# Optimization experiments

Hardware: AMD Instinct MI355X
Metric: run time of the kernel (lower is better)

## Reference

```python
import jax, jax.numpy as jnp
import numpy as np

D_MODEL = 1024
N_HEADS = 16
D_K = D_MODEL // N_HEADS
CAUSAL = True


def setup_inputs() -> dict:
    key = jax.random.key(0)
    ks = jax.random.split(key, 11)
    B, S, D = 2, 2048, D_MODEL
    scale = 1.0 / np.sqrt(D)
    inp = {
        "in_Q": jax.random.normal(ks[0], (B, S, D), jnp.float32),
        "in_K": jax.random.normal(ks[1], (B, S, D), jnp.float32),
        "in_V": jax.random.normal(ks[2], (B, S, D), jnp.float32),
        # torch Linear params: weight [out, in], bias [out]
        "Wq": jax.random.normal(ks[3], (D, D), jnp.float32) * scale,
        "bq": jax.random.normal(ks[4], (D,), jnp.float32) * scale,
        "Wk": jax.random.normal(ks[5], (D, D), jnp.float32) * scale,
        "bk": jax.random.normal(ks[6], (D,), jnp.float32) * scale,
        "Wv": jax.random.normal(ks[7], (D, D), jnp.float32) * scale,
        "bv": jax.random.normal(ks[8], (D,), jnp.float32) * scale,
        "Wo": jax.random.normal(ks[9], (D, D), jnp.float32) * scale,
        "bo": jax.random.normal(ks[10], (D,), jnp.float32) * scale,
    }
    return inp


def reference(in_Q, in_K, in_V, Wq, bq, Wk, bk, Wv, bv, Wo, bo):
    B, S, D = in_Q.shape
    H, dk = N_HEADS, D_K
    # Linear projections (torch: x @ W.T + b)
    Q = in_Q @ Wq.T + bq
    K = in_K @ Wk.T + bk
    V = in_V @ Wv.T + bv
    # split heads: [B, S, D] -> [B, H, S, dk]
    Qh = Q.reshape(B, S, H, dk).transpose(0, 2, 1, 3)
    Kh = K.reshape(B, S, H, dk).transpose(0, 2, 1, 3)
    Vh = V.reshape(B, S, H, dk).transpose(0, 2, 1, 3)
    # scores [B, H, S, S]
    scores = jnp.einsum("bhqd,bhkd->bhqk", Qh, Kh) / jnp.sqrt(jnp.float32(dk))
    if CAUSAL:
        mask = jnp.tril(jnp.ones((S, S), dtype=bool))
        scores = jnp.where(mask, scores, -jnp.inf)
    attn = jax.nn.softmax(scores, axis=-1)
    out = jnp.einsum("bhqk,bhkd->bhqd", attn, Vh)
    Hcat = out.transpose(0, 2, 1, 3).reshape(B, S, D)
    return Hcat @ Wo.T + bo
```

## Files before the change

kernel.cpp:

```cpp
#include <hip/hip_runtime.h>
#include <hip/hip_bf16.h>
#include <math.h>

#define D_MODEL 1024
#define NHEADS  16
#define DK      64
#define SEQ     2048
#define BATCH   2
#define MROWS   4096
#define NQT     (SEQ/64)

typedef unsigned short ushort_t;
using short8 = __attribute__((ext_vector_type(8))) short;
using f32x4  = __attribute__((ext_vector_type(4))) float;

__device__ __forceinline__ ushort_t f2bf(float x) {
    unsigned u = __float_as_uint(x);
    u = (u + 0x7FFFu + ((u >> 16) & 1u)) >> 16;
    return (ushort_t)u;
}

__device__ __forceinline__ unsigned pk2(float a, float b) {
    __hip_bfloat162 h = __float22bfloat162_rn(float2{a, b});
    unsigned u;
    __builtin_memcpy(&u, &h, 4);
    return u;
}

__device__ __forceinline__ void gll16(const ushort_t* g, ushort_t* l) {
    __builtin_amdgcn_global_load_lds(
        (const __attribute__((address_space(1))) void*)(g),
        (__attribute__((address_space(3))) void*)(l), 16, 0, 0);
}

__global__ __launch_bounds__(256) void cvt_bf16(
    const float* s0, const float* s1, const float* s2, const float* s3,
    const float* s4, const float* s5, const float* s6,
    ushort_t* d0, ushort_t* d1, ushort_t* d2, ushort_t* d3,
    ushort_t* d4, ushort_t* d5, ushort_t* d6, int nIn, int nW)
{
    const float* s; ushort_t* d; int n;
    switch (blockIdx.y) {
        case 0: s = s0; d = d0; n = nIn; break;
        case 1: s = s1; d = d1; n = nIn; break;
        case 2: s = s2; d = d2; n = nIn; break;
        case 3: s = s3; d = d3; n = nW;  break;
        case 4: s = s4; d = d4; n = nW;  break;
        case 5: s = s5; d = d5; n = nW;  break;
        default: s = s6; d = d6; n = nW; break;
    }
    int i = (blockIdx.x * 256 + threadIdx.x) * 4;
    if (i < n) {
        float4 v = *(const float4*)&s[i];
        ushort4 o;
        o.x = f2bf(v.x); o.y = f2bf(v.y); o.z = f2bf(v.z); o.w = f2bf(v.w);
        *(ushort4*)&d[i] = o;
    }
}

struct GemmArgs { const ushort_t* A; const ushort_t* W; const float* bias;
                  void* C; int mode; float oscale; };

template<int MODE>
__device__ __forceinline__ void gemm_core(const GemmArgs& ga,
                                          ushort_t* As, ushort_t* Bs)
{
    constexpr bool SWP = (MODE != 1);
    const int tid  = threadIdx.x;
    const int w    = tid >> 6, lane = tid & 63;
    const int quad = lane >> 4, lx = lane & 15;
    const int mw = (w >> 1) * 64, nw = (w & 1) * 64;
    const int bm = blockIdx.x * 128, bn = blockIdx.y * 128;
    const int K = D_MODEL;

    f32x4 acc[4][4];
#pragma unroll
    for (int mt = 0; mt < 4; ++mt)
#pragma unroll
        for (int nt = 0; nt < 4; ++nt)
            acc[mt][nt] = (f32x4){0.f, 0.f, 0.f, 0.f};

    float4 b4[4];
    float  bfr[4];
#pragma unroll
    for (int nt = 0; nt < 4; ++nt) {
        if (SWP) b4[nt] = *(const float4*)&ga.bias[bn + nw + nt * 16 + quad * 4];
        else     bfr[nt] = ga.bias[bn + nw + nt * 16 + lx];
    }

    for (int k0 = 0; k0 < K; k0 += 64) {
        __syncthreads();
#pragma unroll
        for (int i = 0; i < 4; ++i) {
            int r0 = (w * 4 + i) * 8;
            int rl = r0 + (lane >> 3);
            int g  = (lane & 7) ^ (rl & 7);
            gll16(&ga.A[(size_t)(bm + rl) * K + k0 + g * 8], &As[r0 * 64]);
            gll16(&ga.W[(size_t)(bn + rl) * K + k0 + g * 8], &Bs[r0 * 64]);
        }
        __syncthreads();

#pragma unroll
        for (int ks = 0; ks < 2; ++ks) {
            short8 af[4], bf[4];
#pragma unroll
            for (int mt = 0; mt < 4; ++mt) {
                int r = mw + mt * 16 + lx;
                af[mt] = *(const short8*)&As[r * 64 + (((ks * 4 + quad) ^ (r & 7)) << 3)];
            }
#pragma unroll
            for (int nt = 0; nt < 4; ++nt) {
                int r = nw + nt * 16 + lx;
                bf[nt] = *(const short8*)&Bs[r * 64 + (((ks * 4 + quad) ^ (r & 7)) << 3)];
            }
#pragma unroll
            for (int mt = 0; mt < 4; ++mt)
#pragma unroll
                for (int nt = 0; nt < 4; ++nt)
                    acc[mt][nt] = SWP
                        ? __builtin_amdgcn_mfma_f32_16x16x32_bf16(bf[nt], af[mt], acc[mt][nt], 0, 0, 0)
                        : __builtin_amdgcn_mfma_f32_16x16x32_bf16(af[mt], bf[nt], acc[mt][nt], 0, 0, 0);
        }
    }

    if (MODE == 0) {
        ushort_t* C = (ushort_t*)ga.C;
        const float os = ga.oscale;
#pragma unroll
        for (int mt = 0; mt < 4; ++mt) {
            int m = bm + mw + mt * 16 + lx;
#pragma unroll
            for (int nt = 0; nt < 4; ++nt) {
                int n0 = bn + nw + nt * 16 + quad * 4;
                uint2 u;
                u.x = pk2((acc[mt][nt][0] + b4[nt].x) * os, (acc[mt][nt][1] + b4[nt].y) * os);
                u.y = pk2((acc[mt][nt][2] + b4[nt].z) * os, (acc[mt][nt][3] + b4[nt].w) * os);
                *(uint2*)&C[(size_t)m * D_MODEL + n0] = u;
            }
        }
    } else if (MODE == 2) {
        float* C = (float*)ga.C;
#pragma unroll
        for (int mt = 0; mt < 4; ++mt) {
            int m = bm + mw + mt * 16 + lx;
#pragma unroll
            for (int nt = 0; nt < 4; ++nt) {
                int n0 = bn + nw + nt * 16 + quad * 4;
                float4 v;
                v.x = acc[mt][nt][0] + b4[nt].x;
                v.y = acc[mt][nt][1] + b4[nt].y;
                v.z = acc[mt][nt][2] + b4[nt].z;
                v.w = acc[mt][nt][3] + b4[nt].w;
                *(float4*)&C[(size_t)m * D_MODEL + n0] = v;
            }
        }
    } else {
        ushort_t* C = (ushort_t*)ga.C;
#pragma unroll
        for (int mt = 0; mt < 4; ++mt)
#pragma unroll
            for (int nt = 0; nt < 4; ++nt) {
                int n = bn + nw + nt * 16 + lx;
                int d = n & 63, h = n >> 6;
                int m0 = bm + mw + mt * 16 + quad * 4;
                int b = m0 >> 11, s0 = m0 & 2047;
                uint2 u;
                u.x = pk2(acc[mt][nt][0] + bfr[nt], acc[mt][nt][1] + bfr[nt]);
                u.y = pk2(acc[mt][nt][2] + bfr[nt], acc[mt][nt][3] + bfr[nt]);
                *(uint2*)&C[((size_t)(b * NHEADS + h) * DK + d) * SEQ + s0] = u;
            }
    }
}

__global__ __launch_bounds__(256) void gemm_mfma(GemmArgs g0, GemmArgs g1, GemmArgs g2)
{
    __shared__ ushort_t As[128 * 64];
    __shared__ ushort_t Bs[128 * 64];
    GemmArgs ga = (blockIdx.z == 0) ? g0 : ((blockIdx.z == 1) ? g1 : g2);
    if (ga.mode == 0)      gemm_core<0>(ga, As, Bs);
    else if (ga.mode == 1) gemm_core<1>(ga, As, Bs);
    else                   gemm_core<2>(ga, As, Bs);
}

__device__ __forceinline__ void flash_tile(
    int qt, const size_t qbase, const size_t vbase,
    const ushort_t* __restrict__ Qp, const ushort_t* __restrict__ Kp,
    const ushort_t* __restrict__ Vt, ushort_t* __restrict__ Hc,
    ushort_t* Ks, ushort_t* Vs, ushort_t (*Ps)[16 * 72])
{
    const int tid  = threadIdx.x;
    const int w    = tid >> 6, lane = tid & 63;
    const int quad = lane >> 4, lx = lane & 15;

    short8 qf[2];
    {
        size_t ro = qbase + (size_t)(qt * 64 + w * 16 + lx) * D_MODEL + quad * 8;
        qf[0] = *(const short8*)&Qp[ro];
        qf[1] = *(const short8*)&Qp[ro + 32];
    }

    f32x4 O[4];
#pragma unroll
    for (int nt = 0; nt < 4; ++nt) O[nt] = (f32x4){0.f, 0.f, 0.f, 0.f};
    float mrow = -INFINITY, lrow = 0.f;
    const int qin = w * 16 + lx;

    for (int kt = 0; kt <= qt; ++kt) {
        __syncthreads();
#pragma unroll
        for (int i = 0; i < 2; ++i) {
            int r0 = (w + i * 4) * 8;
            int rl = r0 + (lane >> 3);
            int g  = (lane & 7) ^ (rl & 7);
            gll16(&Kp[qbase + (size_t)(kt * 64 + rl) * D_MODEL + g * 8], &Ks[r0 * 64]);
            gll16(&Vt[vbase + (size_t)rl * SEQ + kt * 64 + g * 8], &Vs[r0 * 64]);
        }
        __syncthreads();

        f32x4 s[4];
#pragma unroll
        for (int nt = 0; nt < 4; ++nt) {
            int r = nt * 16 + lx;
            short8 kf0 = *(const short8*)&Ks[r * 64 + ((quad ^ (r & 7)) << 3)];
            short8 kf1 = *(const short8*)&Ks[r * 64 + (((4 + quad) ^ (r & 7)) << 3)];
            f32x4 z = (f32x4){0.f, 0.f, 0.f, 0.f};
            z = __builtin_amdgcn_mfma_f32_16x16x32_bf16(kf0, qf[0], z, 0, 0, 0);
            z = __builtin_amdgcn_mfma_f32_16x16x32_bf16(kf1, qf[1], z, 0, 0, 0);
            s[nt] = z;
        }

        if (kt == qt) {
#pragma unroll
            for (int nt = 0; nt < 4; ++nt)
#pragma unroll
                for (int r = 0; r < 4; ++r)
                    if ((nt * 16 + quad * 4 + r) > qin) s[nt][r] = -INFINITY;
        }

        float tm = -INFINITY;
#pragma unroll
        for (int nt = 0; nt < 4; ++nt)
#pragma unroll
            for (int r = 0; r < 4; ++r) tm = fmaxf(tm, s[nt][r]);
        tm = fmaxf(tm, __shfl_xor(tm, 16, 64));
        tm = fmaxf(tm, __shfl_xor(tm, 32, 64));
        float mnew = fmaxf(mrow, tm);
        float alpha = __builtin_amdgcn_exp2f(mrow - mnew);
        mrow = mnew;
        float rs = 0.f;
#pragma unroll
        for (int nt = 0; nt < 4; ++nt)
#pragma unroll
            for (int r = 0; r < 4; ++r) {
                float p = __builtin_amdgcn_exp2f(s[nt][r] - mnew);
                s[nt][r] = p;
                rs += p;
            }
        rs += __shfl_xor(rs, 16, 64);
        rs += __shfl_xor(rs, 32, 64);
        lrow = lrow * alpha + rs;
#pragma unroll
        for (int nt = 0; nt < 4; ++nt)
#pragma unroll
            for (int r = 0; r < 4; ++r) O[nt][r] *= alpha;

#pragma unroll
        for (int nt = 0; nt < 4; ++nt) {
            uint2 u;
            u.x = pk2(s[nt][0], s[nt][1]);
            u.y = pk2(s[nt][2], s[nt][3]);
            *(uint2*)&Ps[w][lx * 72 + nt * 16 + quad * 4] = u;
        }

        short8 pf0 = *(const short8*)&Ps[w][lx * 72 + quad * 8];
        short8 pf1 = *(const short8*)&Ps[w][lx * 72 + 32 + quad * 8];

#pragma unroll
        for (int nt = 0; nt < 4; ++nt) {
            int r = nt * 16 + lx;
            short8 vf0 = *(const short8*)&Vs[r * 64 + ((quad ^ (r & 7)) << 3)];
            short8 vf1 = *(const short8*)&Vs[r * 64 + (((4 + quad) ^ (r & 7)) << 3)];
            O[nt] = __builtin_amdgcn_mfma_f32_16x16x32_bf16(vf0, pf0, O[nt], 0, 0, 0);
            O[nt] = __builtin_amdgcn_mfma_f32_16x16x32_bf16(vf1, pf1, O[nt], 0, 0, 0);
        }
    }

    {
        float invl = 1.f / lrow;
        size_t ro = qbase + (size_t)(qt * 64 + w * 16 + lx) * D_MODEL;
#pragma unroll
        for (int nt = 0; nt < 4; ++nt) {
            uint2 u;
            u.x = pk2(O[nt][0] * invl, O[nt][1] * invl);
            u.y = pk2(O[nt][2] * invl, O[nt][3] * invl);
            *(uint2*)&Hc[ro + nt * 16 + quad * 4] = u;
        }
    }
}

__global__ __launch_bounds__(256) void flash_mfma(
    const ushort_t* __restrict__ Qp, const ushort_t* __restrict__ Kp,
    const ushort_t* __restrict__ Vt, ushort_t* __restrict__ Hc)
{
    const int p  = blockIdx.x;
    const int bh = blockIdx.y;
    const int b = bh >> 4, h = bh & 15;

    __shared__ ushort_t Ks[64 * 64];
    __shared__ ushort_t Vs[64 * 64];
    __shared__ ushort_t Ps[4][16 * 72];

    const size_t qbase = (size_t)(b * SEQ) * D_MODEL + h * DK;
    const size_t vbase = (size_t)bh * DK * SEQ;

    flash_tile(NQT - 1 - p, qbase, vbase, Qp, Kp, Vt, Hc, Ks, Vs, Ps);
    flash_tile(p,           qbase, vbase, Qp, Kp, Vt, Hc, Ks, Vs, Ps);
}

extern "C" void kernel_launch(void* const* d_in, const int* in_sizes, int n_in,
                              void* d_out, int out_size, void* d_ws, size_t ws_size,
                              hipStream_t stream) {
    const float* inQ = (const float*)d_in[0];
    const float* inK = (const float*)d_in[1];
    const float* inV = (const float*)d_in[2];
    const float* Wq  = (const float*)d_in[3];
    const float* bq  = (const float*)d_in[4];
    const float* Wk  = (const float*)d_in[5];
    const float* bk  = (const float*)d_in[6];
    const float* Wv  = (const float*)d_in[7];
    const float* bv  = (const float*)d_in[8];
    const float* Wo  = (const float*)d_in[9];
    const float* bo  = (const float*)d_in[10];
    float* out = (float*)d_out;

    const size_t NI = (size_t)MROWS * D_MODEL;
    const size_t NW = (size_t)D_MODEL * D_MODEL;
    ushort_t* ws  = (ushort_t*)d_ws;
    ushort_t* Qb  = ws;
    ushort_t* Kb  = Qb  + NI;
    ushort_t* Vb  = Kb  + NI;
    ushort_t* Wqb = Vb  + NI;
    ushort_t* Wkb = Wqb + NW;
    ushort_t* Wvb = Wkb + NW;
    ushort_t* Wob = Wvb + NW;
    ushort_t* Qp  = Wob + NW;
    ushort_t* Kp  = Qp  + NI;
    ushort_t* Vtg = Kp  + NI;
    ushort_t* Hc  = Vtg + NI;

    cvt_bf16<<<dim3(NI / 1024, 7), 256, 0, stream>>>(
        inQ, inK, inV, Wq, Wk, Wv, Wo,
        Qb, Kb, Vb, Wqb, Wkb, Wvb, Wob, (int)NI, (int)NW);

    const float qsc = 0.125f * 1.44269504088896340736f;
    GemmArgs aq{Qb, Wqb, bq, (void*)Qp, 0, qsc};
    GemmArgs ak{Kb, Wkb, bk, (void*)Kp, 0, 1.0f};
    GemmArgs av{Vb, Wvb, bv, (void*)Vtg, 1, 1.0f};
    gemm_mfma<<<dim3(MROWS / 128, D_MODEL / 128, 3), 256, 0, stream>>>(aq, ak, av);

    flash_mfma<<<dim3(NQT / 2, BATCH * NHEADS), 256, 0, stream>>>(Qp, Kp, Vtg, Hc);

    GemmArgs ao{Hc, Wob, bo, (void*)out, 2, 1.0f};
    gemm_mfma<<<dim3(MROWS / 128, D_MODEL / 128, 1), 256, 0, stream>>>(ao, ao, ao);
}
```

Before: 232.2 us.

## Double-buffer K/V tiles in flash attention to prefetch next tile during compute

```diff
diff --git a/kernel.cpp b/kernel.cpp
--- a/kernel.cpp
+++ b/kernel.cpp
@@ -186,11 +186,25 @@
     int qt, const size_t qbase, const size_t vbase,
     const ushort_t* __restrict__ Qp, const ushort_t* __restrict__ Kp,
     const ushort_t* __restrict__ Vt, ushort_t* __restrict__ Hc,
-    ushort_t* Ks, ushort_t* Vs, ushort_t (*Ps)[16 * 72])
+    ushort_t* Ks0, ushort_t* Ks1, ushort_t* Vs0, ushort_t* Vs1,
+    ushort_t (*Ps)[16 * 72])
 {
     const int tid  = threadIdx.x;
     const int w    = tid >> 6, lane = tid & 63;
     const int quad = lane >> 4, lx = lane & 15;
+
+    asm volatile("s_barrier" ::: "memory");
+
+    {
+#pragma unroll
+        for (int i = 0; i < 2; ++i) {
+            int r0 = (w + i * 4) * 8;
+            int rl = r0 + (lane >> 3);
+            int g  = (lane & 7) ^ (rl & 7);
+            gll16(&Kp[qbase + (size_t)(0 * 64 + rl) * D_MODEL + g * 8], &Ks0[r0 * 64]);
+            gll16(&Vt[vbase + (size_t)rl * SEQ + 0 * 64 + g * 8], &Vs0[r0 * 64]);
+        }
+    }
 
     short8 qf[2];
     {
@@ -206,16 +220,24 @@
     const int qin = w * 16 + lx;
 
     for (int kt = 0; kt <= qt; ++kt) {
-        __syncthreads();
-#pragma unroll
-        for (int i = 0; i < 2; ++i) {
-            int r0 = (w + i * 4) * 8;
-            int rl = r0 + (lane >> 3);
-            int g  = (lane & 7) ^ (rl & 7);
-            gll16(&Kp[qbase + (size_t)(kt * 64 + rl) * D_MODEL + g * 8], &Ks[r0 * 64]);
-            gll16(&Vt[vbase + (size_t)rl * SEQ + kt * 64 + g * 8], &Vs[r0 * 64]);
-        }
-        __syncthreads();
+        ushort_t* Ks = (kt & 1) ? Ks1 : Ks0;
+        ushort_t* Vs = (kt & 1) ? Vs1 : Vs0;
+
+        asm volatile("s_waitcnt vmcnt(0)" ::: "memory");
+        asm volatile("s_barrier" ::: "memory");
+
+        if (kt < qt) {
+            ushort_t* Kn = (kt & 1) ? Ks0 : Ks1;
+            ushort_t* Vn = (kt & 1) ? Vs0 : Vs1;
+#pragma unroll
+            for (int i = 0; i < 2; ++i) {
+                int r0 = (w + i * 4) * 8;
+                int rl = r0 + (lane >> 3);
+                int g  = (lane & 7) ^ (rl & 7);
+                gll16(&Kp[qbase + (size_t)((kt + 1) * 64 + rl) * D_MODEL + g * 8], &Kn[r0 * 64]);
+                gll16(&Vt[vbase + (size_t)rl * SEQ + (kt + 1) * 64 + g * 8], &Vn[r0 * 64]);
+            }
+        }
 
         f32x4 s[4];
 #pragma unroll
@@ -306,15 +328,15 @@
     const int bh = blockIdx.y;
     const int b = bh >> 4, h = bh & 15;
 
-    __shared__ ushort_t Ks[64 * 64];
-    __shared__ ushort_t Vs[64 * 64];
+    __shared__ ushort_t Ks0[64 * 64], Ks1[64 * 64];
+    __shared__ ushort_t Vs0[64 * 64], Vs1[64 * 64];
     __shared__ ushort_t Ps[4][16 * 72];
 
     const size_t qbase = (size_t)(b * SEQ) * D_MODEL + h * DK;
     const size_t vbase = (size_t)bh * DK * SEQ;
 
-    flash_tile(NQT - 1 - p, qbase, vbase, Qp, Kp, Vt, Hc, Ks, Vs, Ps);
-    flash_tile(p,           qbase, vbase, Qp, Kp, Vt, Hc, Ks, Vs, Ps);
+    flash_tile(NQT - 1 - p, qbase, vbase, Qp, Kp, Vt, Hc, Ks0, Ks1, Vs0, Vs1, Ps);
+    flash_tile(p,           qbase, vbase, Qp, Kp, Vt, Hc, Ks0, Ks1, Vs0, Vs1, Ps);
 }
 
 extern "C" void kernel_launch(void* const* d_in, const int* in_sizes, int n_in,
```

Result: faster. 226.1 us (-2.7%).
